# Kernel tuning notes

Measured on AMD Instinct MI355X. Metric: run time of the kernel, lower is better.

## Reference

```python
import jax, jax.numpy as jnp
import numpy as np
import math

T, B, D = 1024, 256, 64
E, H, L = 512, 256, 4


def setup_inputs() -> dict:
    key = jax.random.key(0)
    ks = jax.random.split(key, 10)
    x_sequence = jax.random.normal(ks[0], (T, B, D), dtype=jnp.float32)
    seq_lengths = jax.random.randint(ks[1], (B,), 1, T)
    # create_b_mask: ones in first half of dims, zeros in second half
    b_mask = jnp.concatenate([jnp.ones((1, D // 2)), jnp.zeros((1, D // 2))], axis=1).astype(jnp.float32)
    W_in = jax.random.normal(ks[2], (L, D + E, H), dtype=jnp.float32) / np.sqrt(D + E)
    b_in = jnp.zeros((L, H), dtype=jnp.float32)
    W_s = jax.random.normal(ks[3], (L, H, D), dtype=jnp.float32) / np.sqrt(H)
    b_s = jnp.zeros((L, D), dtype=jnp.float32)
    W_t = jax.random.normal(ks[4], (L, H, D), dtype=jnp.float32) / np.sqrt(H)
    b_t = jnp.zeros((L, D), dtype=jnp.float32)
    rescale_w = jnp.ones((1, D), dtype=jnp.float32)
    # ESN reservoir (fixed random), scaled for spectral stability under tanh
    W_res = jax.random.normal(ks[5], (E, E), dtype=jnp.float32) * (0.9 / np.sqrt(E))
    W_inp = jax.random.normal(ks[6], (D, E), dtype=jnp.float32) * 0.1
    return dict(x_sequence=x_sequence, seq_lengths=seq_lengths, b_mask=b_mask,
                W_in=W_in, b_in=b_in, W_s=W_s, b_s=b_s, W_t=W_t, b_t=b_t,
                rescale_w=rescale_w, W_res=W_res, W_inp=W_inp)


def _forward(x_sequence, seq_lengths, b_mask, W_in, b_in, W_s, b_s, W_t, b_t,
             rescale_w, W_res, W_inp):
    Tlen, Bsz, Dd = x_sequence.shape
    log2pi = jnp.asarray(math.log(2.0 * math.pi), dtype=x_sequence.dtype)

    def nn_apply(xm, h_esn, l):
        # small conditioning MLP: concat(masked frame, esn state) -> hidden -> (slope, intercept)
        inp = jnp.concatenate([xm, h_esn], axis=1)           # (B, D+E)
        hid = jnp.tanh(inp @ W_in[l] + b_in[l])              # (B, H)
        slope = jnp.tanh(hid @ W_s[l] + b_s[l]) * rescale_w  # (B, D), rescaled
        intercept = hid @ W_t[l] + b_t[l]                    # (B, D)
        return slope, intercept

    def f_inverse(z, m, h_esn, l):
        slope, intercept = nn_apply(m * z, h_esn, l)
        z_new = m * z + (1.0 - m) * ((z - intercept) * jnp.exp(-slope))
        log_det = slope @ (m.T - 1.0)                        # (B, 1)
        return z_new, log_det

    def loglike_frame(x_frame, h_esn):
        ll = jnp.zeros((Bsz, 1), dtype=x_frame.dtype)
        z = x_frame
        for l in reversed(range(L)):  # small fixed loop over flow layers
            z, ld = f_inverse(z, 1.0 - b_mask, h_esn, l)
            ll = ll + ld
            z, ld = f_inverse(z, b_mask, h_esn, l)
            ll = ll + ld
        ll = ll - 0.5 * jnp.sum(z * z, axis=1, keepdims=True) - 0.5 * Dd * log2pi
        return ll

    def step(carry, inp):
        h_esn, ll_seq = carry
        t, x_frame = inp
        lf = loglike_frame(x_frame, h_esn)
        length_mask = (t < seq_lengths).astype(lf.dtype)[:, None]  # (B,1)
        ll_seq = ll_seq + lf * length_mask
        h_esn = jnp.tanh(h_esn @ W_res.T + x_frame @ W_inp)        # ESN update
        return (h_esn, ll_seq), None

    h0 = jnp.zeros((Bsz, W_res.shape[0]), dtype=x_sequence.dtype)
    ll0 = jnp.zeros((Bsz, 1), dtype=x_sequence.dtype)
    ts = jnp.arange(Tlen)
    (h_final, ll_seq), _ = jax.lax.scan(step, (h0, ll0), (ts, x_sequence))
    return ll_seq  # (B, 1)


def reference(x_sequence, seq_lengths, b_mask, W_in, b_in, W_s, b_s, W_t, b_t,
              rescale_w, W_res, W_inp):
    return _forward(x_sequence, seq_lengths, b_mask, W_in, b_in, W_s, b_s,
                    W_t, b_t, rescale_w, W_res, W_inp)
```

## Files before the change

kernel.cpp:

```cpp
#include <hip/hip_runtime.h>

#define T_LEN 1024
#define B_SZ  256
#define D_DIM 64
#define E_DIM 512
#define H_DIM 256

#define SA 552
#define SH 264
#define SF 66
#define ROWB 1152

using short8 = __attribute__((ext_vector_type(8))) short;
using half8  = __attribute__((ext_vector_type(8))) _Float16;
using f32x4  = __attribute__((ext_vector_type(4))) float;
typedef unsigned long long ull;

static __device__ __forceinline__ unsigned short f2bf(float v) {
    unsigned u = __float_as_uint(v);
    u += 0x7FFFu + ((u >> 16) & 1u);
    return (unsigned short)(u >> 16);
}
static __device__ __forceinline__ unsigned short f2h(float v) {
    _Float16 h = (_Float16)v;
    unsigned short u;
    __builtin_memcpy(&u, &h, 2);
    return u;
}
static __device__ __forceinline__ float h2f(unsigned short u) {
    _Float16 h;
    __builtin_memcpy(&h, &u, 2);
    return (float)h;
}
static __device__ __forceinline__ float fast_tanh(float x) {
    x = fminf(15.f, fmaxf(-15.f, x));
    float e = __expf(2.f * x);
    return (e - 1.f) / (e + 1.f);
}
static __device__ __forceinline__ int rswz(int row, int byte_in_row) {
    return row * ROWB + (byte_in_row ^ ((row & 7) << 4));
}

__global__ void prep_kernel(const float* __restrict__ W_in, const float* __restrict__ W_s,
                            const float* __restrict__ W_t, const float* __restrict__ W_res,
                            const float* __restrict__ W_inp, const float* __restrict__ x_seq,
                            unsigned short* __restrict__ W_inF, unsigned short* __restrict__ W_stF,
                            unsigned short* __restrict__ W_packo, unsigned short* __restrict__ x_h) {
    int idx = blockIdx.x * blockDim.x + threadIdx.x;
    int stride = gridDim.x * blockDim.x;
    const int total1 = 8 * 16 * 17 * 64 * 8;
    for (int i = idx; i < total1; i += stride) {
        int j    = i & 7;
        int lane = (i >> 3) & 63;
        int ks   = (i >> 9) % 17;
        int nt   = (i / (512 * 17)) & 15;
        int ls   = i / (512 * 17 * 16);
        int side = ls & 1, l = ls >> 1;
        int n = nt * 16 + (lane & 15);
        int k = ks * 32 + (lane >> 4) * 8 + j;
        int ksrc = (k < 32) ? (side == 0 ? 32 + k : k) : (k + 32);
        W_inF[i] = f2bf(W_in[(l * 576 + ksrc) * H_DIM + n]);
    }
    const int total2 = 8 * 4 * 8 * 64 * 8;
    for (int i = idx; i < total2; i += stride) {
        int j    = i & 7;
        int lane = (i >> 3) & 63;
        int ks   = (i >> 9) & 7;
        int nt   = (i >> 12) & 3;
        int ls   = i >> 14;
        int side = ls & 1, l = ls >> 1;
        int nst = nt * 16 + (lane & 15);
        int k   = ks * 32 + (lane >> 4) * 8 + j;
        int j32 = nst & 31;
        int d   = side ? (32 + j32) : j32;
        float v = (nst < 32) ? W_s[(l * H_DIM + k) * D_DIM + d] : W_t[(l * H_DIM + k) * D_DIM + d];
        W_stF[i] = f2bf(v);
    }
    const int total3 = E_DIM * 576;
    for (int i = idx; i < total3; i += stride) {
        int k = i % 576;
        int n = i / 576;
        float v = (k < E_DIM) ? W_res[n * E_DIM + k] : W_inp[(k - E_DIM) * E_DIM + n];
        W_packo[i] = f2h(v);
    }
    const int total4 = T_LEN * B_SZ * D_DIM;
    for (int i = idx; i < total4; i += stride)
        x_h[i] = f2h(x_seq[i]);
}

__launch_bounds__(256, 1)
__global__ void esn_kernel(const unsigned short* __restrict__ x_h,
                           const unsigned short* __restrict__ W_pack,
                           unsigned short* __restrict__ h_store ,
                           unsigned short* __restrict__ h_buf   ,
                           unsigned int* __restrict__ ctr,
                           int t0, int tc) {
    const int bid  = blockIdx.x;
    const int g    = bid & 15;
    const int m    = bid >> 4;
    const int tid  = threadIdx.x;
    const int wave = tid >> 6;
    const int lane = tid & 63;
    const int arow = lane & 15;
    const int kq   = lane >> 4;
    const int r0   = g * 16;
    const int n0   = m * 64;
    const size_t HB = (size_t)B_SZ * E_DIM;
    unsigned int* gctr = ctr + g * 32;

    extern __shared__ char smem[];
    char* Wlb = smem;
    char* hAb = smem + 64 * ROWB;

    {
        const int r  = tid & 63;
        const int c0 = (tid >> 6) * 18;
        #pragma unroll
        for (int u = 0; u < 18; ++u) {
            const int byte = 16 * (c0 + u);
            *reinterpret_cast<uint4*>(Wlb + rswz(r, byte)) =
                *reinterpret_cast<const uint4*>(
                    reinterpret_cast<const char*>(&W_pack[(size_t)(n0 + r) * 576]) + byte);
        }
    }

    const int srow = tid >> 4;
    const int seg  = tid & 15;
    const int xrow = tid >> 2, xc = tid & 3;

    for (int tl = 0; tl < tc; ++tl) {
        const int t = t0 + tl;
        const unsigned short* hb_r = h_buf + (size_t)(t & 1) * HB;
        unsigned short*       hb_w = h_buf + (size_t)((t & 1) ^ 1) * HB;

        uint4 xa = {0,0,0,0}, xb = {0,0,0,0};
        if (tid < 64) {
            const unsigned short* xp = &x_h[((size_t)t * B_SZ + r0 + xrow) * D_DIM + xc * 16];
            xa = *reinterpret_cast<const uint4*>(xp);
            xb = *reinterpret_cast<const uint4*>(xp + 8);
        }

        if (tid == 0) {
            while (__hip_atomic_fetch_add(gctr, 0u, __ATOMIC_RELAXED,
                                          __HIP_MEMORY_SCOPE_AGENT) < 8u * (unsigned)t)
                __builtin_amdgcn_s_sleep(1);
        }
        __syncthreads();
        asm volatile("" ::: "memory");

        ull hv[8];
        const ull* hrow = reinterpret_cast<const ull*>(&hb_r[(size_t)(r0 + srow) * E_DIM]);
        #pragma unroll
        for (int q = 0; q < 4; ++q) {
            const int c = seg + 16 * q;
            hv[2*q]   = __hip_atomic_load(hrow + 2*c,     __ATOMIC_RELAXED, __HIP_MEMORY_SCOPE_SYSTEM);
            hv[2*q+1] = __hip_atomic_load(hrow + 2*c + 1, __ATOMIC_RELAXED, __HIP_MEMORY_SCOPE_SYSTEM);
        }
        #pragma unroll
        for (int q = 0; q < 4; ++q) {
            const int c = seg + 16 * q;
            uint4 pk;
            __builtin_memcpy(&pk, &hv[2*q], 16);
            *reinterpret_cast<uint4*>(hAb + rswz(srow, 16 * c)) = pk;
        }
        if (tid < 64) {
            *reinterpret_cast<uint4*>(hAb + rswz(xrow, 1024 + 32 * xc))      = xa;
            *reinterpret_cast<uint4*>(hAb + rswz(xrow, 1024 + 32 * xc + 16)) = xb;
        }
        __syncthreads();

        if (tl == 0) {
            #pragma unroll
            for (int q = 0; q < 4; ++q) {
                const int c = seg + 16 * q;
                unsigned short o[8];
                #pragma unroll
                for (int j = 0; j < 4; ++j) o[j]     = f2bf(h2f((unsigned short)(hv[2*q]   >> (16 * j))));
                #pragma unroll
                for (int j = 0; j < 4; ++j) o[4 + j] = f2bf(h2f((unsigned short)(hv[2*q+1] >> (16 * j))));
                uint4 pk;
                __builtin_memcpy(&pk, o, 16);
                *reinterpret_cast<uint4*>(&h_store[(size_t)(r0 + srow) * E_DIM + 8 * c]) = pk;
            }
        }

        f32x4 accA = (f32x4){0.f, 0.f, 0.f, 0.f};
        f32x4 accB = (f32x4){0.f, 0.f, 0.f, 0.f};
        #pragma unroll
        for (int ks = 0; ks < 18; ++ks) {
            half8 a = *reinterpret_cast<const half8*>(hAb + rswz(arow, ks * 64 + kq * 16));
            half8 b = *reinterpret_cast<const half8*>(Wlb + rswz(wave * 16 + arow, ks * 64 + kq * 16));
            if (ks & 1) accB = __builtin_amdgcn_mfma_f32_16x16x32_f16(a, b, accB, 0, 0, 0);
            else        accA = __builtin_amdgcn_mfma_f32_16x16x32_f16(a, b, accA, 0, 0, 0);
        }
        f32x4 acc = accA + accB;

        const int ncol = n0 + wave * 16 + arow;
        #pragma unroll
        for (int i = 0; i < 4; ++i) {
            const int row = r0 + kq * 4 + i;
            float hvf = fast_tanh(acc[i]);
            __hip_atomic_store(&hb_w[(size_t)row * E_DIM + ncol], f2h(hvf),
                               __ATOMIC_RELAXED, __HIP_MEMORY_SCOPE_SYSTEM);
            if (tl + 1 < tc)
                h_store[((size_t)(tl + 1) * B_SZ + row) * E_DIM + ncol] = f2bf(hvf);
        }

        asm volatile("s_waitcnt vmcnt(0)" ::: "memory");
        __syncthreads();
        if (tid == 0)
            __hip_atomic_fetch_add(gctr, 1u, __ATOMIC_RELAXED, __HIP_MEMORY_SCOPE_AGENT);
    }
}

__launch_bounds__(256, 2)
__global__ void flow_kernel(const float* __restrict__ x_seq, const unsigned short* __restrict__ h_store,
                            const unsigned short* __restrict__ W_inF, const unsigned short* __restrict__ W_stF,
                            const float* __restrict__ b_in, const float* __restrict__ b_s,
                            const float* __restrict__ b_t, const float* __restrict__ rescale_w,
                            const int* __restrict__ seq_len, float* __restrict__ ll_part,
                            int t0, int tc) {
    const int tt   = blockIdx.x >> 4;
    const int bt   = blockIdx.x & 15;
    const int tid  = threadIdx.x;
    const int wave = tid >> 6;
    const int lane = tid & 63;

    __shared__ unsigned short abf[32 * SA];
    __shared__ unsigned short hidbf[32 * SH];
    __shared__ float zf[32][D_DIM];
    __shared__ float llacc[32];
    __shared__ float llb[16];
    float* stf = reinterpret_cast<float*>(hidbf);

    if (tid < 16) llb[tid] = 0.f;

    const int r8 = tid >> 3;
    const int c8 = tid & 7;

    for (int s = 0; s < 8; ++s) {
        const int trow = tt * 16 + 2 * s + (r8 >> 4);
        const int brow = bt * 16 + (r8 & 15);
        {
            const float* xp = &x_seq[((size_t)(t0 + trow) * B_SZ + brow) * D_DIM + c8 * 8];
            float4 v0 = *reinterpret_cast<const float4*>(xp);
            float4 v1 = *reinterpret_cast<const float4*>(xp + 4);
            *reinterpret_cast<float4*>(&zf[r8][c8 * 8])     = v0;
            *reinterpret_cast<float4*>(&zf[r8][c8 * 8 + 4]) = v1;
            const unsigned short* hp = &h_store[((size_t)trow * B_SZ + brow) * E_DIM + c8 * 64];
            unsigned short* ap = &abf[r8 * SA + 32 + c8 * 64];
            #pragma unroll
            for (int q = 0; q < 8; ++q)
                *reinterpret_cast<uint4*>(ap + q * 8) = *reinterpret_cast<const uint4*>(hp + q * 8);
        }
        if (tid < 32) llacc[tid] = 0.f;
        __syncthreads();

        for (int stage = 0; stage < 8; ++stage) {
            const int l = 3 - (stage >> 1);
            const int side = stage & 1;
            const int ls = l * 2 + side;
            {
                #pragma unroll
                for (int q = 0; q < 4; ++q) {
                    int k = c8 * 4 + q;
                    int d = side ? k : (32 + k);
                    abf[r8 * SA + k] = f2bf(zf[r8][d]);
                }
            }
            __syncthreads();

            const unsigned short* wbase =
                W_inF + ((size_t)(ls * 16 + wave * 4) * 17) * 512 + lane * 8;
            f32x4 acc[2][4];
            #pragma unroll
            for (int mt = 0; mt < 2; ++mt)
                #pragma unroll
                for (int nt = 0; nt < 4; ++nt)
                    acc[mt][nt] = (f32x4){0.f, 0.f, 0.f, 0.f};
            const int aoff = (lane & 15) * SA + 8 * (lane >> 4);
            short8 bb[6][4];
            #pragma unroll
            for (int p = 0; p < 6; ++p)
                #pragma unroll
                for (int nt = 0; nt < 4; ++nt)
                    bb[p][nt] = *reinterpret_cast<const short8*>(wbase + (size_t)nt * 8704 + p * 512);
            #pragma unroll
            for (int ks = 0; ks < 17; ++ks) {
                const int k0 = ks * 32;
                short8 a0 = *reinterpret_cast<const short8*>(&abf[aoff + k0]);
                short8 a1 = *reinterpret_cast<const short8*>(&abf[16 * SA + aoff + k0]);
                #pragma unroll
                for (int nt = 0; nt < 4; ++nt) {
                    acc[0][nt] = __builtin_amdgcn_mfma_f32_16x16x32_bf16(a0, bb[ks % 6][nt], acc[0][nt], 0, 0, 0);
                    acc[1][nt] = __builtin_amdgcn_mfma_f32_16x16x32_bf16(a1, bb[ks % 6][nt], acc[1][nt], 0, 0, 0);
                }
                if (ks + 6 < 17) {
                    #pragma unroll
                    for (int nt = 0; nt < 4; ++nt)
                        bb[ks % 6][nt] = *reinterpret_cast<const short8*>(
                            wbase + (size_t)nt * 8704 + (ks + 6) * 512);
                }
            }
            #pragma unroll
            for (int mt = 0; mt < 2; ++mt)
                #pragma unroll
                for (int nt = 0; nt < 4; ++nt) {
                    const int n = wave * 64 + nt * 16 + (lane & 15);
                    const float bias = b_in[l * H_DIM + n];
                    #pragma unroll
                    for (int i = 0; i < 4; ++i) {
                        const int row = mt * 16 + (lane >> 4) * 4 + i;
                        hidbf[row * SH + n] = f2bf(fast_tanh(acc[mt][nt][i] + bias));
                    }
                }
            __syncthreads();

            const unsigned short* wstb =
                W_stF + ((size_t)(ls * 4 + wave) * 8) * 512 + lane * 8;
            f32x4 acc2[2];
            acc2[0] = (f32x4){0.f,0.f,0.f,0.f};
            acc2[1] = (f32x4){0.f,0.f,0.f,0.f};
            const int hoff = (lane & 15) * SH + 8 * (lane >> 4);
            const int nst  = wave * 16 + (lane & 15);
            short8 bs0 = *reinterpret_cast<const short8*>(wstb);
            #pragma unroll
            for (int ks = 0; ks < 8; ++ks) {
                short8 bcur = bs0;
                if (ks + 1 < 8) bs0 = *reinterpret_cast<const short8*>(wstb + (ks + 1) * 512);
                const int k0 = ks * 32;
                short8 a0 = *reinterpret_cast<const short8*>(&hidbf[hoff + k0]);
                short8 a1 = *reinterpret_cast<const short8*>(&hidbf[16 * SH + hoff + k0]);
                acc2[0] = __builtin_amdgcn_mfma_f32_16x16x32_bf16(a0, bcur, acc2[0], 0, 0, 0);
                acc2[1] = __builtin_amdgcn_mfma_f32_16x16x32_bf16(a1, bcur, acc2[1], 0, 0, 0);
            }
            __syncthreads();
            {
                const int j = nst & 31;
                const int d = side ? (32 + j) : j;
                const bool is_s = (nst < 32);
                const float bias = is_s ? b_s[l * D_DIM + d] : b_t[l * D_DIM + d];
                const float rs = rescale_w[d];
                #pragma unroll
                for (int mt = 0; mt < 2; ++mt)
                    #pragma unroll
                    for (int i = 0; i < 4; ++i) {
                        const int row = mt * 16 + (lane >> 4) * 4 + i;
                        const float v = acc2[mt][i] + bias;
                        stf[row * SF + nst] = is_s ? (fast_tanh(v) * rs) : v;
                    }
            }
            __syncthreads();
            {
                float p = 0.f;
                #pragma unroll
                for (int q = 0; q < 4; ++q) {
                    const int j = c8 * 4 + q;
                    const int d = side ? (32 + j) : j;
                    const float sv = stf[r8 * SF + j];
                    const float iv = stf[r8 * SF + 32 + j];
                    zf[r8][d] = (zf[r8][d] - iv) * __expf(-sv);
                    p += sv;
                }
                p += __shfl_xor(p, 1);
                p += __shfl_xor(p, 2);
                p += __shfl_xor(p, 4);
                if (c8 == 0) llacc[r8] -= p;
            }
            __syncthreads();
        }

        {
            float zs = 0.f;
            #pragma unroll
            for (int q = 0; q < 8; ++q) {
                float z = zf[r8][c8 * 8 + q];
                zs += z * z;
            }
            zs += __shfl_xor(zs, 1);
            zs += __shfl_xor(zs, 2);
            zs += __shfl_xor(zs, 4);
            if (c8 == 0) {
                float ll = llacc[r8] - 0.5f * zs - 58.812066125f;
                llacc[r8] = ((t0 + trow) < seq_len[brow]) ? ll : 0.f;
            }
        }
        __syncthreads();
        if (tid < 16) llb[tid] += llacc[tid] + llacc[16 + tid];
        __syncthreads();
    }

    if (tid < 16)
        ll_part[((t0 >> 4) + tt) * B_SZ + bt * 16 + tid] = llb[tid];
}

__global__ void reduce_kernel(const float* __restrict__ ll_part, float* __restrict__ out) {
    int b = threadIdx.x;
    float s = 0.f;
    #pragma unroll
    for (int tt = 0; tt < T_LEN / 16; ++tt) s += ll_part[tt * B_SZ + b];
    out[b] = s;
}

extern "C" void kernel_launch(void* const* d_in, const int* in_sizes, int n_in,
                              void* d_out, int out_size, void* d_ws, size_t ws_size,
                              hipStream_t stream) {
    const float* x_seq   = (const float*)d_in[0];
    const int*   seqlen  = (const int*)d_in[1];
    const float* W_in    = (const float*)d_in[3];
    const float* b_in    = (const float*)d_in[4];
    const float* W_s     = (const float*)d_in[5];
    const float* b_s     = (const float*)d_in[6];
    const float* W_t     = (const float*)d_in[7];
    const float* b_t     = (const float*)d_in[8];
    const float* rescale = (const float*)d_in[9];
    const float* W_res   = (const float*)d_in[10];
    const float* W_inp   = (const float*)d_in[11];

    char* ws = (char*)d_ws;
    size_t off = 0;
    unsigned short* W_inF  = (unsigned short*)(ws + off); off += (size_t)8 * 16 * 17 * 64 * 8 * 2;
    unsigned short* W_stF  = (unsigned short*)(ws + off); off += (size_t)8 * 4 * 8 * 64 * 8 * 2;
    unsigned short* W_pack = (unsigned short*)(ws + off); off += (size_t)E_DIM * 576 * 2;
    unsigned short* x_h    = (unsigned short*)(ws + off); off += (size_t)T_LEN * B_SZ * D_DIM * 2;
    float* ll_part = (float*)(ws + off); off += (size_t)(T_LEN / 16) * B_SZ * 4;
    unsigned short* h_buf  = (unsigned short*)(ws + off); off += (size_t)2 * B_SZ * E_DIM * 2;
    unsigned int* ctr = (unsigned int*)(ws + off); off += (size_t)16 * 32 * 4;
    unsigned short* h_store = (unsigned short*)(ws + off);

    size_t per_t = (size_t)B_SZ * E_DIM * 2;
    size_t rem = (ws_size > off) ? (ws_size - off) : 0;
    long long tcl = (long long)(rem / per_t);
    int tc = (int)((tcl > T_LEN) ? T_LEN : tcl);
    tc &= ~15;
    if (tc < 16) tc = 16;

    hipMemsetAsync(h_buf, 0, (size_t)2 * B_SZ * E_DIM * 2, stream);
    hipMemsetAsync(ctr, 0, (size_t)16 * 32 * 4, stream);

    prep_kernel<<<2048, 256, 0, stream>>>(W_in, W_s, W_t, W_res, W_inp, x_seq,
                                          W_inF, W_stF, W_pack, x_h);
    const int esn_lds = (64 + 16) * ROWB;
    for (int t0 = 0; t0 < T_LEN; t0 += tc) {
        int cur = T_LEN - t0; if (cur > tc) cur = tc;
        esn_kernel<<<128, 256, esn_lds, stream>>>(x_h, W_pack, h_store, h_buf, ctr, t0, cur);
        flow_kernel<<<(cur / 16) * 16, 256, 0, stream>>>(x_seq, h_store, W_inF, W_stF, b_in, b_s, b_t,
                                                         rescale, seqlen, ll_part, t0, cur);
    }
    reduce_kernel<<<1, B_SZ, 0, stream>>>(ll_part, (float*)d_out);
}
```

Before: 3.851 ms.

## Fuse ESN and flow kernels to overlap chunks via double-buffered h_store

Merges the ESN recurrence and flow-likelihood kernels into one launch whose first 128 blocks run the sequential ESN for the current time chunk, while the remaining blocks process the flow MLP for the previous chunk. h_store is double-buffered in chunks of up to 128 steps, so the two phases overlap instead of serialising. The ESN h_store write is also moved after the barrier arrive to shorten the critical path. The risk is that flow blocks compete with the latency-bound ESN blocks for CUs and bandwidth. The chunking also adds more launches and a final flow-only launch.

Result: slower. 4.249 ms (+10.3%).

```diff
diff --git a/kernel.cpp b/kernel.cpp
--- a/kernel.cpp
+++ b/kernel.cpp
@@ -10,6 +10,9 @@
 #define SH 264
 #define SF 66
 #define ROWB 1152
+
+#define ESN_LDS  (80 * ROWB)
+#define FLOW_LDS (32*SA*2 + 32*SH*2 + 32*64*4 + 32*4 + 16*4)
 
 using short8 = __attribute__((ext_vector_type(8))) short;
 using half8  = __attribute__((ext_vector_type(8))) _Float16;
@@ -89,309 +92,336 @@
 }
 
 __launch_bounds__(256, 1)
-__global__ void esn_kernel(const unsigned short* __restrict__ x_h,
-                           const unsigned short* __restrict__ W_pack,
-                           unsigned short* __restrict__ h_store ,
-                           unsigned short* __restrict__ h_buf   ,
-                           unsigned int* __restrict__ ctr,
-                           int t0, int tc) {
-    const int bid  = blockIdx.x;
-    const int g    = bid & 15;
-    const int m    = bid >> 4;
-    const int tid  = threadIdx.x;
+__global__ void fused_kernel(const unsigned short* __restrict__ x_h,
+                             const unsigned short* __restrict__ W_pack,
+                             unsigned short* __restrict__ hse ,
+                             unsigned short* __restrict__ h_buf ,
+                             unsigned int* __restrict__ ctr,
+                             int t0e, int tce,
+                             const float* __restrict__ x_seq,
+                             const unsigned short* __restrict__ hsf ,
+                             const unsigned short* __restrict__ W_inF,
+                             const unsigned short* __restrict__ W_stF,
+                             const float* __restrict__ b_in, const float* __restrict__ b_s,
+                             const float* __restrict__ b_t, const float* __restrict__ rescale_w,
+                             const int* __restrict__ seq_len, float* __restrict__ ll_part,
+                             int t0f, int tcf) {
+    extern __shared__ char smem[];
+    const int ebn = (tce > 0) ? 128 : 0;
+    const int tid = threadIdx.x;
     const int wave = tid >> 6;
     const int lane = tid & 63;
-    const int arow = lane & 15;
-    const int kq   = lane >> 4;
-    const int r0   = g * 16;
-    const int n0   = m * 64;
-    const size_t HB = (size_t)B_SZ * E_DIM;
-    unsigned int* gctr = ctr + g * 32;
-
-    extern __shared__ char smem[];
-    char* Wlb = smem;
-    char* hAb = smem + 64 * ROWB;
-
-    {
-        const int r  = tid & 63;
-        const int c0 = (tid >> 6) * 18;
-        #pragma unroll
-        for (int u = 0; u < 18; ++u) {
-            const int byte = 16 * (c0 + u);
-            *reinterpret_cast<uint4*>(Wlb + rswz(r, byte)) =
-                *reinterpret_cast<const uint4*>(
-                    reinterpret_cast<const char*>(&W_pack[(size_t)(n0 + r) * 576]) + byte);
+
+    if ((int)blockIdx.x < ebn) {
+        const int bid  = blockIdx.x;
+        const int g    = bid & 15;
+        const int m    = bid >> 4;
+        const int arow = lane & 15;
+        const int kq   = lane >> 4;
+        const int r0   = g * 16;
+        const int n0   = m * 64;
+        const size_t HB = (size_t)B_SZ * E_DIM;
+        unsigned int* gctr = ctr + g * 32;
+
+        char* Wlb = smem;
+        char* hAb = smem + 64 * ROWB;
+
+        {
+            const int r  = tid & 63;
+            const int c0 = (tid >> 6) * 18;
+            #pragma unroll
+            for (int u = 0; u < 18; ++u) {
+                const int byte = 16 * (c0 + u);
+                *reinterpret_cast<uint4*>(Wlb + rswz(r, byte)) =
+                    *reinterpret_cast<const uint4*>(
+                        reinterpret_cast<const char*>(&W_pack[(size_t)(n0 + r) * 576]) + byte);
+            }
         }
-    }
-
-    const int srow = tid >> 4;
-    const int seg  = tid & 15;
-    const int xrow = tid >> 2, xc = tid & 3;
-
-    for (int tl = 0; tl < tc; ++tl) {
-        const int t = t0 + tl;
-        const unsigned short* hb_r = h_buf + (size_t)(t & 1) * HB;
-        unsigned short*       hb_w = h_buf + (size_t)((t & 1) ^ 1) * HB;
-
-        uint4 xa = {0,0,0,0}, xb = {0,0,0,0};
-        if (tid < 64) {
-            const unsigned short* xp = &x_h[((size_t)t * B_SZ + r0 + xrow) * D_DIM + xc * 16];
-            xa = *reinterpret_cast<const uint4*>(xp);
-            xb = *reinterpret_cast<const uint4*>(xp + 8);
-        }
-
-        if (tid == 0) {
-            while (__hip_atomic_fetch_add(gctr, 0u, __ATOMIC_RELAXED,
-                                          __HIP_MEMORY_SCOPE_AGENT) < 8u * (unsigned)t)
-                __builtin_amdgcn_s_sleep(1);
-        }
-        __syncthreads();
-        asm volatile("" ::: "memory");
-
-        ull hv[8];
-        const ull* hrow = reinterpret_cast<const ull*>(&hb_r[(size_t)(r0 + srow) * E_DIM]);
-        #pragma unroll
-        for (int q = 0; q < 4; ++q) {
-            const int c = seg + 16 * q;
-            hv[2*q]   = __hip_atomic_load(hrow + 2*c,     __ATOMIC_RELAXED, __HIP_MEMORY_SCOPE_SYSTEM);
-            hv[2*q+1] = __hip_atomic_load(hrow + 2*c + 1, __ATOMIC_RELAXED, __HIP_MEMORY_SCOPE_SYSTEM);
-        }
-        #pragma unroll
-        for (int q = 0; q < 4; ++q) {
-            const int c = seg + 16 * q;
-            uint4 pk;
-            __builtin_memcpy(&pk, &hv[2*q], 16);
-            *reinterpret_cast<uint4*>(hAb + rswz(srow, 16 * c)) = pk;
-        }
-        if (tid < 64) {
-            *reinterpret_cast<uint4*>(hAb + rswz(xrow, 1024 + 32 * xc))      = xa;
-            *reinterpret_cast<uint4*>(hAb + rswz(xrow, 1024 + 32 * xc + 16)) = xb;
-        }
-        __syncthreads();
-
-        if (tl == 0) {
+
+        const int srow = tid >> 4;
+        const int seg  = tid & 15;
+        const int xrow = tid >> 2, xc = tid & 3;
+
+        for (int tl = 0; tl < tce; ++tl) {
+            const int t = t0e + tl;
+            const unsigned short* hb_r = h_buf + (size_t)(t & 1) * HB;
+            unsigned short*       hb_w = h_buf + (size_t)((t & 1) ^ 1) * HB;
+
+            uint4 xa = {0,0,0,0}, xb = {0,0,0,0};
+            if (tid < 64) {
+                const unsigned short* xp = &x_h[((size_t)t * B_SZ + r0 + xrow) * D_DIM + xc * 16];
+                xa = *reinterpret_cast<const uint4*>(xp);
+                xb = *reinterpret_cast<const uint4*>(xp + 8);
+            }
+
+            if (tid == 0) {
+                while (__hip_atomic_fetch_add(gctr, 0u, __ATOMIC_RELAXED,
+                                              __HIP_MEMORY_SCOPE_AGENT) < 8u * (unsigned)t)
+                    __builtin_amdgcn_s_sleep(1);
+            }
+            __syncthreads();
+            asm volatile("" ::: "memory");
+
+            ull hv[8];
+            const ull* hrow = reinterpret_cast<const ull*>(&hb_r[(size_t)(r0 + srow) * E_DIM]);
             #pragma unroll
             for (int q = 0; q < 4; ++q) {
                 const int c = seg + 16 * q;
-                unsigned short o[8];
-                #pragma unroll
-                for (int j = 0; j < 4; ++j) o[j]     = f2bf(h2f((unsigned short)(hv[2*q]   >> (16 * j))));
-                #pragma unroll
-                for (int j = 0; j < 4; ++j) o[4 + j] = f2bf(h2f((unsigned short)(hv[2*q+1] >> (16 * j))));
+                hv[2*q]   = __hip_atomic_load(hrow + 2*c,     __ATOMIC_RELAXED, __HIP_MEMORY_SCOPE_SYSTEM);
+                hv[2*q+1] = __hip_atomic_load(hrow + 2*c + 1, __ATOMIC_RELAXED, __HIP_MEMORY_SCOPE_SYSTEM);
+            }
+            #pragma unroll
+            for (int q = 0; q < 4; ++q) {
+                const int c = seg + 16 * q;
                 uint4 pk;
-                __builtin_memcpy(&pk, o, 16);
-                *reinterpret_cast<uint4*>(&h_store[(size_t)(r0 + srow) * E_DIM + 8 * c]) = pk;
+                __builtin_memcpy(&pk, &hv[2*q], 16);
+                *reinterpret_cast<uint4*>(hAb + rswz(srow, 16 * c)) = pk;
+            }
+            if (tid < 64) {
+                *reinterpret_cast<uint4*>(hAb + rswz(xrow, 1024 + 32 * xc))      = xa;
+                *reinterpret_cast<uint4*>(hAb + rswz(xrow, 1024 + 32 * xc + 16)) = xb;
+            }
+            __syncthreads();
+
+            if (tl == 0) {
+                #pragma unroll
+                for (int q = 0; q < 4; ++q) {
+                    const int c = seg + 16 * q;
+                    unsigned short o[8];
+                    #pragma unroll
+                    for (int j = 0; j < 4; ++j) o[j]     = f2bf(h2f((unsigned short)(hv[2*q]   >> (16 * j))));
+                    #pragma unroll
+                    for (int j = 0; j < 4; ++j) o[4 + j] = f2bf(h2f((unsigned short)(hv[2*q+1] >> (16 * j))));
+                    uint4 pk;
+                    __builtin_memcpy(&pk, o, 16);
+                    *reinterpret_cast<uint4*>(&hse[(size_t)(r0 + srow) * E_DIM + 8 * c]) = pk;
+                }
+            }
+
+            f32x4 accA = (f32x4){0.f, 0.f, 0.f, 0.f};
+            f32x4 accB = (f32x4){0.f, 0.f, 0.f, 0.f};
+            #pragma unroll
+            for (int ks = 0; ks < 18; ++ks) {
+                half8 a = *reinterpret_cast<const half8*>(hAb + rswz(arow, ks * 64 + kq * 16));
+                half8 b = *reinterpret_cast<const half8*>(Wlb + rswz(wave * 16 + arow, ks * 64 + kq * 16));
+                if (ks & 1) accB = __builtin_amdgcn_mfma_f32_16x16x32_f16(a, b, accB, 0, 0, 0);
+                else        accA = __builtin_amdgcn_mfma_f32_16x16x32_f16(a, b, accA, 0, 0, 0);
+            }
+            f32x4 acc = accA + accB;
+
+            const int ncol = n0 + wave * 16 + arow;
+            float hsv[8];
+            #pragma unroll
+            for (int nt = 0; nt < 2; ++nt)
+                #pragma unroll
+                for (int i = 0; i < 4; ++i) {
+                    const int row = r0 + kq * 4 + i;
+                    float hvf = fast_tanh(acc[nt * 4 + i < 4 ? i : i]);
+                    (void)hvf;
+                }
+            {
+                #pragma unroll
+                for (int i = 0; i < 4; ++i) {
+                    const int row = r0 + kq * 4 + i;
+                    float h0 = fast_tanh(acc[i]);
+                    (void)row; (void)h0;
+                }
+            }
+            #pragma unroll
+            for (int i = 0; i < 4; ++i) {
+                const int row = r0 + kq * 4 + i;
+                float hvf = fast_tanh(acc[i]);
+                hsv[i] = hvf;
+                __hip_atomic_store(&hb_w[(size_t)row * E_DIM + ncol], f2h(hvf),
+                                   __ATOMIC_RELAXED, __HIP_MEMORY_SCOPE_SYSTEM);
+            }
+
+            asm volatile("s_waitcnt vmcnt(0)" ::: "memory");
+            __syncthreads();
+            if (tid == 0)
+                __hip_atomic_fetch_add(gctr, 1u, __ATOMIC_RELAXED, __HIP_MEMORY_SCOPE_AGENT);
+
+            if (tl + 1 < tce) {
+                #pragma unroll
+                for (int i = 0; i < 4; ++i) {
+                    const int row = r0 + kq * 4 + i;
+                    hse[((size_t)(tl + 1) * B_SZ + row) * E_DIM + ncol] = f2bf(hsv[i]);
+                }
             }
         }
-
-        f32x4 accA = (f32x4){0.f, 0.f, 0.f, 0.f};
-        f32x4 accB = (f32x4){0.f, 0.f, 0.f, 0.f};
-        #pragma unroll
-        for (int ks = 0; ks < 18; ++ks) {
-            half8 a = *reinterpret_cast<const half8*>(hAb + rswz(arow, ks * 64 + kq * 16));
-            half8 b = *reinterpret_cast<const half8*>(Wlb + rswz(wave * 16 + arow, ks * 64 + kq * 16));
-            if (ks & 1) accB = __builtin_amdgcn_mfma_f32_16x16x32_f16(a, b, accB, 0, 0, 0);
-            else        accA = __builtin_amdgcn_mfma_f32_16x16x32_f16(a, b, accA, 0, 0, 0);
-        }
-        f32x4 acc = accA + accB;
-
-        const int ncol = n0 + wave * 16 + arow;
-        #pragma unroll
-        for (int i = 0; i < 4; ++i) {
-            const int row = r0 + kq * 4 + i;
-            float hvf = fast_tanh(acc[i]);
-            __hip_atomic_store(&hb_w[(size_t)row * E_DIM + ncol], f2h(hvf),
-                               __ATOMIC_RELAXED, __HIP_MEMORY_SCOPE_SYSTEM);
-            if (tl + 1 < tc)
-                h_store[((size_t)(tl + 1) * B_SZ + row) * E_DIM + ncol] = f2bf(hvf);
-        }
-
-        asm volatile("s_waitcnt vmcnt(0)" ::: "memory");
-        __syncthreads();
-        if (tid == 0)
-            __hip_atomic_fetch_add(gctr, 1u, __ATOMIC_RELAXED, __HIP_MEMORY_SCOPE_AGENT);
-    }
-}
-
-__launch_bounds__(256, 2)
-__global__ void flow_kernel(const float* __restrict__ x_seq, const unsigned short* __restrict__ h_store,
-                            const unsigned short* __restrict__ W_inF, const unsigned short* __restrict__ W_stF,
-                            const float* __restrict__ b_in, const float* __restrict__ b_s,
-                            const float* __restrict__ b_t, const float* __restrict__ rescale_w,
-                            const int* __restrict__ seq_len, float* __restrict__ ll_part,
-                            int t0, int tc) {
-    const int tt   = blockIdx.x >> 4;
-    const int bt   = blockIdx.x & 15;
-    const int tid  = threadIdx.x;
-    const int wave = tid >> 6;
-    const int lane = tid & 63;
-
-    __shared__ unsigned short abf[32 * SA];
-    __shared__ unsigned short hidbf[32 * SH];
-    __shared__ float zf[32][D_DIM];
-    __shared__ float llacc[32];
-    __shared__ float llb[16];
-    float* stf = reinterpret_cast<float*>(hidbf);
-
-    if (tid < 16) llb[tid] = 0.f;
-
-    const int r8 = tid >> 3;
-    const int c8 = tid & 7;
-
-    for (int s = 0; s < 8; ++s) {
-        const int trow = tt * 16 + 2 * s + (r8 >> 4);
-        const int brow = bt * 16 + (r8 & 15);
-        {
-            const float* xp = &x_seq[((size_t)(t0 + trow) * B_SZ + brow) * D_DIM + c8 * 8];
-            float4 v0 = *reinterpret_cast<const float4*>(xp);
-            float4 v1 = *reinterpret_cast<const float4*>(xp + 4);
-            *reinterpret_cast<float4*>(&zf[r8][c8 * 8])     = v0;
-            *reinterpret_cast<float4*>(&zf[r8][c8 * 8 + 4]) = v1;
-            const unsigned short* hp = &h_store[((size_t)trow * B_SZ + brow) * E_DIM + c8 * 64];
-            unsigned short* ap = &abf[r8 * SA + 32 + c8 * 64];
-            #pragma unroll
-            for (int q = 0; q < 8; ++q)
-                *reinterpret_cast<uint4*>(ap + q * 8) = *reinterpret_cast<const uint4*>(hp + q * 8);
-        }
-        if (tid < 32) llacc[tid] = 0.f;
-        __syncthreads();
-
-        for (int stage = 0; stage < 8; ++stage) {
-            const int l = 3 - (stage >> 1);
-            const int side = stage & 1;
-            const int ls = l * 2 + side;
+    } else {
+        if (tcf <= 0) return;
+        const int fbid = (int)blockIdx.x - ebn;
+        const int tt   = fbid >> 4;
+        const int bt   = fbid & 15;
+
+        unsigned short* abf   = reinterpret_cast<unsigned short*>(smem);
+        unsigned short* hidbf = abf + 32 * SA;
+        float* zf    = reinterpret_cast<float*>(hidbf + 32 * SH);
+        float* llacc = zf + 32 * 64;
+        float* llb   = llacc + 32;
+        float* stf   = reinterpret_cast<float*>(hidbf);
+
+        if (tid < 16) llb[tid] = 0.f;
+
+        const int r8 = tid >> 3;
+        const int c8 = tid & 7;
+
+        for (int s = 0; s < 8; ++s) {
+            const int trow = tt * 16 + 2 * s + (r8 >> 4);
+            const int brow = bt * 16 + (r8 & 15);
             {
-                #pragma unroll
-                for (int q = 0; q < 4; ++q) {
-                    int k = c8 * 4 + q;
-                    int d = side ? k : (32 + k);
-                    abf[r8 * SA + k] = f2bf(zf[r8][d]);
-                }
-            }
+                const float* xp = &x_seq[((size_t)(t0f + trow) * B_SZ + brow) * D_DIM + c8 * 8];
+                float4 v0 = *reinterpret_cast<const float4*>(xp);
+                float4 v1 = *reinterpret_cast<const float4*>(xp + 4);
+                *reinterpret_cast<float4*>(&zf[r8 * 64 + c8 * 8])     = v0;
+                *reinterpret_cast<float4*>(&zf[r8 * 64 + c8 * 8 + 4]) = v1;
+                const unsigned short* hp = &hsf[((size_t)trow * B_SZ + brow) * E_DIM + c8 * 64];
+                unsigned short* ap = &abf[r8 * SA + 32 + c8 * 64];
+                #pragma unroll
+                for (int q = 0; q < 8; ++q)
+                    *reinterpret_cast<uint4*>(ap + q * 8) = *reinterpret_cast<const uint4*>(hp + q * 8);
+            }
+            if (tid < 32) llacc[tid] = 0.f;
             __syncthreads();
 
-            const unsigned short* wbase =
-                W_inF + ((size_t)(ls * 16 + wave * 4) * 17) * 512 + lane * 8;
-            f32x4 acc[2][4];
-            #pragma unroll
-            for (int mt = 0; mt < 2; ++mt)
-                #pragma unroll
-                for (int nt = 0; nt < 4; ++nt)
-                    acc[mt][nt] = (f32x4){0.f, 0.f, 0.f, 0.f};
-            const int aoff = (lane & 15) * SA + 8 * (lane >> 4);
-            short8 bb[6][4];
-            #pragma unroll
-            for (int p = 0; p < 6; ++p)
-                #pragma unroll
-                for (int nt = 0; nt < 4; ++nt)
-                    bb[p][nt] = *reinterpret_cast<const short8*>(wbase + (size_t)nt * 8704 + p * 512);
-            #pragma unroll
-            for (int ks = 0; ks < 17; ++ks) {
-                const int k0 = ks * 32;
-                short8 a0 = *reinterpret_cast<const short8*>(&abf[aoff + k0]);
-                short8 a1 = *reinterpret_cast<const short8*>(&abf[16 * SA + aoff + k0]);
-                #pragma unroll
-                for (int nt = 0; nt < 4; ++nt) {
-                    acc[0][nt] = __builtin_amdgcn_mfma_f32_16x16x32_bf16(a0, bb[ks % 6][nt], acc[0][nt], 0, 0, 0);
-                    acc[1][nt] = __builtin_amdgcn_mfma_f32_16x16x32_bf16(a1, bb[ks % 6][nt], acc[1][nt], 0, 0, 0);
-                }
-                if (ks + 6 < 17) {
+            for (int stage = 0; stage < 8; ++stage) {
+                const int l = 3 - (stage >> 1);
+                const int side = stage & 1;
+                const int ls = l * 2 + side;
+                {
+                    #pragma unroll
+                    for (int q = 0; q < 4; ++q) {
+                        int k = c8 * 4 + q;
+                        int d = side ? k : (32 + k);
+                        abf[r8 * SA + k] = f2bf(zf[r8 * 64 + d]);
+                    }
+                }
+                __syncthreads();
+
+                const unsigned short* wbase =
+                    W_inF + ((size_t)(ls * 16 + wave * 4) * 17) * 512 + lane * 8;
+                f32x4 acc[2][4];
+                #pragma unroll
+                for (int mt = 0; mt < 2; ++mt)
                     #pragma unroll
                     for (int nt = 0; nt < 4; ++nt)
-                        bb[ks % 6][nt] = *reinterpret_cast<const short8*>(
-                            wbase + (size_t)nt * 8704 + (ks + 6) * 512);
-                }
-            }
-            #pragma unroll
-            for (int mt = 0; mt < 2; ++mt)
-                #pragma unroll
-                for (int nt = 0; nt < 4; ++nt) {
-                    const int n = wave * 64 + nt * 16 + (lane & 15);
-                    const float bias = b_in[l * H_DIM + n];
-                    #pragma unroll
-                    for (int i = 0; i < 4; ++i) {
-                        const int row = mt * 16 + (lane >> 4) * 4 + i;
-                        hidbf[row * SH + n] = f2bf(fast_tanh(acc[mt][nt][i] + bias));
+                        acc[mt][nt] = (f32x4){0.f, 0.f, 0.f, 0.f};
+                const int aoff = (lane & 15) * SA + 8 * (lane >> 4);
+                short8 bb[6][4];
+                #pragma unroll
+                for (int p = 0; p < 6; ++p)
+                    #pragma unroll
+                    for (int nt = 0; nt < 4; ++nt)
+                        bb[p][nt] = *reinterpret_cast<const short8*>(wbase + (size_t)nt * 8704 + p * 512);
+                #pragma unroll
+                for (int ks = 0; ks < 17; ++ks) {
+                    const int k0 = ks * 32;
+                    short8 a0 = *reinterpret_cast<const short8*>(&abf[aoff + k0]);
+                    short8 a1 = *reinterpret_cast<const short8*>(&abf[16 * SA + aoff + k0]);
+                    #pragma unroll
+                    for (int nt = 0; nt < 4; ++nt) {
+                        acc[0][nt] = __builtin_amdgcn_mfma_f32_16x16x32_bf16(a0, bb[ks % 6][nt], acc[0][nt], 0, 0, 0);
+                        acc[1][nt] = __builtin_amdgcn_mfma_f32_16x16x32_bf16(a1, bb[ks % 6][nt], acc[1][nt], 0, 0, 0);
                     }
-                }
+                    if (ks + 6 < 17) {
+                        #pragma unroll
+                        for (int nt = 0; nt < 4; ++nt)
+                            bb[ks % 6][nt] = *reinterpret_cast<const short8*>(
+                                wbase + (size_t)nt * 8704 + (ks + 6) * 512);
+                    }
+                }
+                #pragma unroll
+                for (int mt = 0; mt < 2; ++mt)
+                    #pragma unroll
+                    for (int nt = 0; nt < 4; ++nt) {
+                        const int n = wave * 64 + nt * 16 + (lane & 15);
+                        const float bias = b_in[l * H_DIM + n];
+                        #pragma unroll
+                        for (int i = 0; i < 4; ++i) {
+                            const int row = mt * 16 + (lane >> 4) * 4 + i;
+                            hidbf[row * SH + n] = f2bf(fast_tanh(acc[mt][nt][i] + bias));
+                        }
+                    }
+                __syncthreads();
+
+                const unsigned short* wstb =
+                    W_stF + ((size_t)(ls * 4 + wave) * 8) * 512 + lane * 8;
+                f32x4 acc2[2];
+                acc2[0] = (f32x4){0.f,0.f,0.f,0.f};
+                acc2[1] = (f32x4){0.f,0.f,0.f,0.f};
+                const int hoff = (lane & 15) * SH + 8 * (lane >> 4);
+                const int nst  = wave * 16 + (lane & 15);
+                short8 bs0 = *reinterpret_cast<const short8*>(wstb);
+                #pragma unroll
+                for (int ks = 0; ks < 8; ++ks) {
+                    short8 bcur = bs0;
+                    if (ks + 1 < 8) bs0 = *reinterpret_cast<const short8*>(wstb + (ks + 1) * 512);
+                    const int k0 = ks * 32;
+                    short8 a0 = *reinterpret_cast<const short8*>(&hidbf[hoff + k0]);
+                    short8 a1 = *reinterpret_cast<const short8*>(&hidbf[16 * SH + hoff + k0]);
+                    acc2[0] = __builtin_amdgcn_mfma_f32_16x16x32_bf16(a0, bcur, acc2[0], 0, 0, 0);
+                    acc2[1] = __builtin_amdgcn_mfma_f32_16x16x32_bf16(a1, bcur, acc2[1], 0, 0, 0);
+                }
+                __syncthreads();
+                {
+                    const int j = nst & 31;
+                    const int d = side ? (32 + j) : j;
+                    const bool is_s = (nst < 32);
+                    const float bias = is_s ? b_s[l * D_DIM + d] : b_t[l * D_DIM + d];
+                    const float rs = rescale_w[d];
+                    #pragma unroll
+                    for (int mt = 0; mt < 2; ++mt)
+                        #pragma unroll
+                        for (int i = 0; i < 4; ++i) {
+                            const int row = mt * 16 + (lane >> 4) * 4 + i;
+                            const float v = acc2[mt][i] + bias;
+                            stf[row * SF + nst] = is_s ? (fast_tanh(v) * rs) : v;
+                        }
+                }
+                __syncthreads();
+                {
+                    float p = 0.f;
+                    #pragma unroll
+                    for (int q = 0; q < 4; ++q) {
+                        const int j = c8 * 4 + q;
+                        const int d = side ? (32 + j) : j;
+                        const float sv = stf[r8 * SF + j];
+                        const float iv = stf[r8 * SF + 32 + j];
+                        zf[r8 * 64 + d] = (zf[r8 * 64 + d] - iv) * __expf(-sv);
+                        p += sv;
+                    }
+                    p += __shfl_xor(p, 1);
+                    p += __shfl_xor(p, 2);
+                    p += __shfl_xor(p, 4);
+                    if (c8 == 0) llacc[r8] -= p;
+                }
+                __syncthreads();
+            }
+
+            {
+                float zs = 0.f;
+                #pragma unroll
+                for (int q = 0; q < 8; ++q) {
+                    float z = zf[r8 * 64 + c8 * 8 + q];
+                    zs += z * z;
+                }
+                zs += __shfl_xor(zs, 1);
+                zs += __shfl_xor(zs, 2);
+                zs += __shfl_xor(zs, 4);
+                if (c8 == 0) {
+                    float ll = llacc[r8] - 0.5f * zs - 58.812066125f;
+                    llacc[r8] = ((t0f + trow) < seq_len[brow]) ? ll : 0.f;
+                }
+            }
             __syncthreads();
-
-            const unsigned short* wstb =
-                W_stF + ((size_t)(ls * 4 + wave) * 8) * 512 + lane * 8;
-            f32x4 acc2[2];
-            acc2[0] = (f32x4){0.f,0.f,0.f,0.f};
-            acc2[1] = (f32x4){0.f,0.f,0.f,0.f};
-            const int hoff = (lane & 15) * SH + 8 * (lane >> 4);
-            const int nst  = wave * 16 + (lane & 15);
-            short8 bs0 = *reinterpret_cast<const short8*>(wstb);
-            #pragma unroll
-            for (int ks = 0; ks < 8; ++ks) {
-                short8 bcur = bs0;
-                if (ks + 1 < 8) bs0 = *reinterpret_cast<const short8*>(wstb + (ks + 1) * 512);
-                const int k0 = ks * 32;
-                short8 a0 = *reinterpret_cast<const short8*>(&hidbf[hoff + k0]);
-                short8 a1 = *reinterpret_cast<const short8*>(&hidbf[16 * SH + hoff + k0]);
-                acc2[0] = __builtin_amdgcn_mfma_f32_16x16x32_bf16(a0, bcur, acc2[0], 0, 0, 0);
-                acc2[1] = __builtin_amdgcn_mfma_f32_16x16x32_bf16(a1, bcur, acc2[1], 0, 0, 0);
-            }
-            __syncthreads();
-            {
-                const int j = nst & 31;
-                const int d = side ? (32 + j) : j;
-                const bool is_s = (nst < 32);
-                const float bias = is_s ? b_s[l * D_DIM + d] : b_t[l * D_DIM + d];
-                const float rs = rescale_w[d];
-                #pragma unroll
-                for (int mt = 0; mt < 2; ++mt)
-                    #pragma unroll
-                    for (int i = 0; i < 4; ++i) {
-                        const int row = mt * 16 + (lane >> 4) * 4 + i;
-                        const float v = acc2[mt][i] + bias;
-                        stf[row * SF + nst] = is_s ? (fast_tanh(v) * rs) : v;
-                    }
-            }
-            __syncthreads();
-            {
-                float p = 0.f;
-                #pragma unroll
-                for (int q = 0; q < 4; ++q) {
-                    const int j = c8 * 4 + q;
-                    const int d = side ? (32 + j) : j;
-                    const float sv = stf[r8 * SF + j];
-                    const float iv = stf[r8 * SF + 32 + j];
-                    zf[r8][d] = (zf[r8][d] - iv) * __expf(-sv);
-                    p += sv;
-                }
-                p += __shfl_xor(p, 1);
-                p += __shfl_xor(p, 2);
-                p += __shfl_xor(p, 4);
-                if (c8 == 0) llacc[r8] -= p;
-            }
+            if (tid < 16) llb[tid] += llacc[tid] + llacc[16 + tid];
             __syncthreads();
         }
 
-        {
-            float zs = 0.f;
-            #pragma unroll
-            for (int q = 0; q < 8; ++q) {
-                float z = zf[r8][c8 * 8 + q];
-                zs += z * z;
-            }
-            zs += __shfl_xor(zs, 1);
-            zs += __shfl_xor(zs, 2);
-            zs += __shfl_xor(zs, 4);
-            if (c8 == 0) {
-                float ll = llacc[r8] - 0.5f * zs - 58.812066125f;
-                llacc[r8] = ((t0 + trow) < seq_len[brow]) ? ll : 0.f;
-            }
-        }
-        __syncthreads();
-        if (tid < 16) llb[tid] += llacc[tid] + llacc[16 + tid];
-        __syncthreads();
+        if (tid < 16)
+            ll_part[((t0f >> 4) + tt) * B_SZ + bt * 16 + tid] = llb[tid];
     }
-
-    if (tid < 16)
-        ll_part[((t0 >> 4) + tt) * B_SZ + bt * 16 + tid] = llb[tid];
 }
 
 __global__ void reduce_kernel(const float* __restrict__ ll_part, float* __restrict__ out) {
@@ -426,26 +456,55 @@
     float* ll_part = (float*)(ws + off); off += (size_t)(T_LEN / 16) * B_SZ * 4;
     unsigned short* h_buf  = (unsigned short*)(ws + off); off += (size_t)2 * B_SZ * E_DIM * 2;
     unsigned int* ctr = (unsigned int*)(ws + off); off += (size_t)16 * 32 * 4;
-    unsigned short* h_store = (unsigned short*)(ws + off);
-
-    size_t per_t = (size_t)B_SZ * E_DIM * 2;
+    unsigned short* hs_base = (unsigned short*)(ws + off);
+
+    const size_t per_t = (size_t)B_SZ * E_DIM * 2;
     size_t rem = (ws_size > off) ? (ws_size - off) : 0;
-    long long tcl = (long long)(rem / per_t);
-    int tc = (int)((tcl > T_LEN) ? T_LEN : tcl);
-    tc &= ~15;
-    if (tc < 16) tc = 16;
 
     hipMemsetAsync(h_buf, 0, (size_t)2 * B_SZ * E_DIM * 2, stream);
     hipMemsetAsync(ctr, 0, (size_t)16 * 32 * 4, stream);
-
     prep_kernel<<<2048, 256, 0, stream>>>(W_in, W_s, W_t, W_res, W_inp, x_seq,
                                           W_inF, W_stF, W_pack, x_h);
-    const int esn_lds = (64 + 16) * ROWB;
-    for (int t0 = 0; t0 < T_LEN; t0 += tc) {
-        int cur = T_LEN - t0; if (cur > tc) cur = tc;
-        esn_kernel<<<128, 256, esn_lds, stream>>>(x_h, W_pack, h_store, h_buf, ctr, t0, cur);
-        flow_kernel<<<(cur / 16) * 16, 256, 0, stream>>>(x_seq, h_store, W_inF, W_stF, b_in, b_s, b_t,
-                                                         rescale, seqlen, ll_part, t0, cur);
+
+    long long tpd = (long long)(rem / (2 * per_t));
+    int tcp = (int)((tpd > 128) ? 128 : tpd);
+    tcp &= ~15;
+
+    if (tcp >= 16) {
+        unsigned short* hs0 = hs_base;
+        unsigned short* hs1 = hs_base + (size_t)tcp * B_SZ * E_DIM;
+        int c = 0, pt0 = 0, pcur = 0;
+        for (int t0 = 0; t0 < T_LEN; t0 += tcp, ++c) {
+            int cur = T_LEN - t0; if (cur > tcp) cur = tcp;
+            unsigned short* hse = (c & 1) ? hs1 : hs0;
+            unsigned short* hsf = (c & 1) ? hs0 : hs1;
+            fused_kernel<<<128 + pcur, 256, ESN_LDS, stream>>>(
+                x_h, W_pack, hse, h_buf, ctr, t0, cur,
+                x_seq, hsf, W_inF, W_stF, b_in, b_s, b_t, rescale, seqlen, ll_part,
+                pt0, pcur);
+            pt0 = t0; pcur = cur;
+        }
+        unsigned short* hsl = ((c - 1) & 1) ? hs1 : hs0;
+        fused_kernel<<<pcur, 256, FLOW_LDS, stream>>>(
+            x_h, W_pack, hs0, h_buf, ctr, 0, 0,
+            x_seq, hsl, W_inF, W_stF, b_in, b_s, b_t, rescale, seqlen, ll_part,
+            pt0, pcur);
+    } else {
+        long long tsd = (long long)(rem / per_t);
+        int tcs = (int)((tsd > T_LEN) ? T_LEN : tsd);
+        tcs &= ~15;
+        if (tcs < 16) tcs = 16;
+        for (int t0 = 0; t0 < T_LEN; t0 += tcs) {
+            int cur = T_LEN - t0; if (cur > tcs) cur = tcs;
+            fused_kernel<<<128, 256, ESN_LDS, stream>>>(
+                x_h, W_pack, hs_base, h_buf, ctr, t0, cur,
+                x_seq, hs_base, W_inF, W_stF, b_in, b_s, b_t, rescale, seqlen, ll_part,
+                0, 0);
+            fused_kernel<<<cur, 256, FLOW_LDS, stream>>>(
+                x_h, W_pack, hs_base, h_buf, ctr, 0, 0,
+                x_seq, hs_base, W_inF, W_stF, b_in, b_s, b_t, rescale, seqlen, ll_part,
+                t0, cur);
+        }
     }
     reduce_kernel<<<1, B_SZ, 0, stream>>>(ll_part, (float*)d_out);
 }
```

## Replace ESN atomic step counter with parity-tagged triple-buffered hidden state

Applied to the files above, without the earlier changes.

Drops the per-group global atomic counter and its spin-wait barrier. Each fp16 hidden value now has its low mantissa bit overwritten with the step parity, and the buffer rotates over three slots. Readers poll each 8-byte chunk until all four lanes carry the expected parity, so a block consumes only the data it needs without a global handshake. This removes the end-of-step vmcnt wait, a __syncthreads and the atomic increment, at the cost of one bit of fp16 precision in the recurrent state and repeated polling loads.

After: 4.538 ms. +17.8%, slower.

```diff
diff --git a/kernel.cpp b/kernel.cpp
--- a/kernel.cpp
+++ b/kernel.cpp
@@ -45,7 +45,8 @@
                             const float* __restrict__ W_t, const float* __restrict__ W_res,
                             const float* __restrict__ W_inp, const float* __restrict__ x_seq,
                             unsigned short* __restrict__ W_inF, unsigned short* __restrict__ W_stF,
-                            unsigned short* __restrict__ W_packo, unsigned short* __restrict__ x_h) {
+                            unsigned short* __restrict__ W_packo, unsigned short* __restrict__ x_h,
+                            unsigned short* __restrict__ h_buf) {
     int idx = blockIdx.x * blockDim.x + threadIdx.x;
     int stride = gridDim.x * blockDim.x;
     const int total1 = 8 * 16 * 17 * 64 * 8;
@@ -86,6 +87,9 @@
     const int total4 = T_LEN * B_SZ * D_DIM;
     for (int i = idx; i < total4; i += stride)
         x_h[i] = f2h(x_seq[i]);
+    const int total5 = B_SZ * E_DIM;
+    for (int i = idx; i < total5; i += stride)
+        h_buf[2 * total5 + i] = 0x0001;
 }
 
 __launch_bounds__(256, 1)
@@ -93,7 +97,6 @@
                            const unsigned short* __restrict__ W_pack,
                            unsigned short* __restrict__ h_store ,
                            unsigned short* __restrict__ h_buf   ,
-                           unsigned int* __restrict__ ctr,
                            int t0, int tc) {
     const int bid  = blockIdx.x;
     const int g    = bid & 15;
@@ -106,7 +109,6 @@
     const int r0   = g * 16;
     const int n0   = m * 64;
     const size_t HB = (size_t)B_SZ * E_DIM;
-    unsigned int* gctr = ctr + g * 32;
 
     extern __shared__ char smem[];
     char* Wlb = smem;
@@ -130,8 +132,10 @@
 
     for (int tl = 0; tl < tc; ++tl) {
         const int t = t0 + tl;
-        const unsigned short* hb_r = h_buf + (size_t)(t & 1) * HB;
-        unsigned short*       hb_w = h_buf + (size_t)((t & 1) ^ 1) * HB;
+        const unsigned pr = (unsigned)(t & 1);
+        const unsigned short pw = (unsigned short)((t + 1) & 1);
+        const unsigned short* hb_r = h_buf + (size_t)(t % 3) * HB;
+        unsigned short*       hb_w = h_buf + (size_t)((t + 1) % 3) * HB;
 
         uint4 xa = {0,0,0,0}, xb = {0,0,0,0};
         if (tid < 64) {
@@ -140,34 +144,39 @@
             xb = *reinterpret_cast<const uint4*>(xp + 8);
         }
 
-        if (tid == 0) {
-            while (__hip_atomic_fetch_add(gctr, 0u, __ATOMIC_RELAXED,
-                                          __HIP_MEMORY_SCOPE_AGENT) < 8u * (unsigned)t)
-                __builtin_amdgcn_s_sleep(1);
-        }
-        __syncthreads();
-        asm volatile("" ::: "memory");
-
+        const ull* hrow = reinterpret_cast<const ull*>(&hb_r[(size_t)(r0 + srow) * E_DIM]);
+        const ull MASK = 0x0001000100010001ULL;
+        const ull WANT = pr ? MASK : 0ULL;
         ull hv[8];
-        const ull* hrow = reinterpret_cast<const ull*>(&hb_r[(size_t)(r0 + srow) * E_DIM]);
-        #pragma unroll
-        for (int q = 0; q < 4; ++q) {
-            const int c = seg + 16 * q;
-            hv[2*q]   = __hip_atomic_load(hrow + 2*c,     __ATOMIC_RELAXED, __HIP_MEMORY_SCOPE_SYSTEM);
-            hv[2*q+1] = __hip_atomic_load(hrow + 2*c + 1, __ATOMIC_RELAXED, __HIP_MEMORY_SCOPE_SYSTEM);
-        }
+        unsigned got = 0;
+        while (got != 0xFFu) {
+            ull tmp[8];
+            #pragma unroll
+            for (int q = 0; q < 8; ++q) {
+                const int w = 2 * (seg + 16 * (q >> 1)) + (q & 1);
+                if (!((got >> q) & 1u))
+                    tmp[q] = __hip_atomic_load(hrow + w, __ATOMIC_RELAXED, __HIP_MEMORY_SCOPE_SYSTEM);
+            }
+            #pragma unroll
+            for (int q = 0; q < 8; ++q) {
+                if (!((got >> q) & 1u) && ((tmp[q] & MASK) == WANT)) {
+                    hv[q] = tmp[q];
+                    got |= 1u << q;
+                }
+            }
+        }
+
         #pragma unroll
         for (int q = 0; q < 4; ++q) {
             const int c = seg + 16 * q;
             uint4 pk;
-            __builtin_memcpy(&pk, &hv[2*q], 16);
+            __builtin_memcpy(&pk, &hv[2 * q], 16);
             *reinterpret_cast<uint4*>(hAb + rswz(srow, 16 * c)) = pk;
         }
         if (tid < 64) {
             *reinterpret_cast<uint4*>(hAb + rswz(xrow, 1024 + 32 * xc))      = xa;
             *reinterpret_cast<uint4*>(hAb + rswz(xrow, 1024 + 32 * xc + 16)) = xb;
         }
-        __syncthreads();
 
         if (tl == 0) {
             #pragma unroll
@@ -183,6 +192,7 @@
                 *reinterpret_cast<uint4*>(&h_store[(size_t)(r0 + srow) * E_DIM + 8 * c]) = pk;
             }
         }
+        __syncthreads();
 
         f32x4 accA = (f32x4){0.f, 0.f, 0.f, 0.f};
         f32x4 accB = (f32x4){0.f, 0.f, 0.f, 0.f};
@@ -200,16 +210,13 @@
         for (int i = 0; i < 4; ++i) {
             const int row = r0 + kq * 4 + i;
             float hvf = fast_tanh(acc[i]);
-            __hip_atomic_store(&hb_w[(size_t)row * E_DIM + ncol], f2h(hvf),
+            unsigned short u = f2h(hvf);
+            u = (unsigned short)((u & 0xFFFEu) | pw);
+            __hip_atomic_store(&hb_w[(size_t)row * E_DIM + ncol], u,
                                __ATOMIC_RELAXED, __HIP_MEMORY_SCOPE_SYSTEM);
             if (tl + 1 < tc)
                 h_store[((size_t)(tl + 1) * B_SZ + row) * E_DIM + ncol] = f2bf(hvf);
         }
-
-        asm volatile("s_waitcnt vmcnt(0)" ::: "memory");
-        __syncthreads();
-        if (tid == 0)
-            __hip_atomic_fetch_add(gctr, 1u, __ATOMIC_RELAXED, __HIP_MEMORY_SCOPE_AGENT);
     }
 }
 
@@ -424,8 +431,7 @@
     unsigned short* W_pack = (unsigned short*)(ws + off); off += (size_t)E_DIM * 576 * 2;
     unsigned short* x_h    = (unsigned short*)(ws + off); off += (size_t)T_LEN * B_SZ * D_DIM * 2;
     float* ll_part = (float*)(ws + off); off += (size_t)(T_LEN / 16) * B_SZ * 4;
-    unsigned short* h_buf  = (unsigned short*)(ws + off); off += (size_t)2 * B_SZ * E_DIM * 2;
-    unsigned int* ctr = (unsigned int*)(ws + off); off += (size_t)16 * 32 * 4;
+    unsigned short* h_buf  = (unsigned short*)(ws + off); off += (size_t)3 * B_SZ * E_DIM * 2;
     unsigned short* h_store = (unsigned short*)(ws + off);
 
     size_t per_t = (size_t)B_SZ * E_DIM * 2;
@@ -435,15 +441,14 @@
     tc &= ~15;
     if (tc < 16) tc = 16;
 
-    hipMemsetAsync(h_buf, 0, (size_t)2 * B_SZ * E_DIM * 2, stream);
-    hipMemsetAsync(ctr, 0, (size_t)16 * 32 * 4, stream);
+    hipMemsetAsync(h_buf, 0, (size_t)3 * B_SZ * E_DIM * 2, stream);
 
     prep_kernel<<<2048, 256, 0, stream>>>(W_in, W_s, W_t, W_res, W_inp, x_seq,
-                                          W_inF, W_stF, W_pack, x_h);
+                                          W_inF, W_stF, W_pack, x_h, h_buf);
     const int esn_lds = (64 + 16) * ROWB;
     for (int t0 = 0; t0 < T_LEN; t0 += tc) {
         int cur = T_LEN - t0; if (cur > tc) cur = tc;
-        esn_kernel<<<128, 256, esn_lds, stream>>>(x_h, W_pack, h_store, h_buf, ctr, t0, cur);
+        esn_kernel<<<128, 256, esn_lds, stream>>>(x_h, W_pack, h_store, h_buf, t0, cur);
         flow_kernel<<<(cur / 16) * 16, 256, 0, stream>>>(x_seq, h_store, W_inF, W_stF, b_in, b_s, b_t,
                                                          rescale, seqlen, ll_part, t0, cur);
     }
```
